# Kernel optimization log

Measured on AMD Instinct MI355X. Metric: run time of the kernel, lower is better.

## Reference

```python
import jax, jax.numpy as jnp
import numpy as np

DIM = 256
HEAD_DIM = 16
HEADS = DIM // HEAD_DIM          # 16
TOTAL = HEADS * HEAD_DIM         # 256
QKV_CH = 3 * TOTAL               # 768
NUM_SCALES = 1
HEADS_TOTAL = HEADS * (1 + NUM_SCALES)  # 32
PROJ_IN = TOTAL * (1 + NUM_SCALES)      # 512
PW_GROUPS = 3 * HEADS            # 48
ATT_EPS = 1e-15
BN_EPS = 1e-5


def _conv(x, w, groups=1, pad=0):
    return jax.lax.conv_general_dilated(
        x, w, window_strides=(1, 1), padding=[(pad, pad), (pad, pad)],
        dimension_numbers=("NCHW", "OIHW", "NCHW"), feature_group_count=groups)


def setup_inputs() -> dict:
    key = jax.random.key(0)
    ks = jax.random.split(key, 9)
    B, H, W = 16, 64, 64
    s = lambda fan: 1.0 / np.sqrt(fan)
    return {
        "x": jax.random.normal(ks[0], (B, DIM, H, W), jnp.float32),
        "w_qkv": jax.random.normal(ks[1], (QKV_CH, DIM, 1, 1), jnp.float32) * s(DIM),
        "w_dw": jax.random.normal(ks[2], (QKV_CH, 1, 5, 5), jnp.float32) * s(25),
        "w_pw": jax.random.normal(ks[3], (QKV_CH, QKV_CH // PW_GROUPS, 1, 1), jnp.float32) * s(QKV_CH // PW_GROUPS),
        "w_proj": jax.random.normal(ks[4], (DIM, PROJ_IN, 1, 1), jnp.float32) * s(PROJ_IN),
        "bn_gamma": jnp.ones((DIM,), jnp.float32),
        "bn_beta": jnp.zeros((DIM,), jnp.float32),
        "bn_mean": jax.random.normal(ks[5], (DIM,), jnp.float32) * 0.1,
        "bn_var": jax.random.uniform(ks[6], (DIM,), jnp.float32, 0.5, 1.5),
    }


def reference(x, w_qkv, w_dw, w_pw, w_proj, bn_gamma, bn_beta, bn_mean, bn_var):
    B, C, H, W = x.shape
    N = H * W
    # qkv projection (1x1 conv, no norm/act)
    qkv = _conv(x, w_qkv)                                   # (B, 768, H, W)
    # multi-scale aggregation: depthwise 5x5 + grouped pointwise
    agg = _conv(_conv(qkv, w_dw, groups=QKV_CH, pad=2), w_pw, groups=PW_GROUPS)
    ms = jnp.concatenate([qkv, agg], axis=1)                # (B, 1536, H, W)
    ms = ms.reshape(B, HEADS_TOTAL, 3 * HEAD_DIM, N)        # (B, 32, 48, N)
    q, k, v = jnp.split(ms, 3, axis=2)                      # each (B, 32, 16, N)
    q = jax.nn.relu(q).astype(jnp.float32)
    k = jax.nn.relu(k).astype(jnp.float32)
    v = v.astype(jnp.float32)
    # pad v with a row of ones -> carries the normalizer through the matmuls
    v_pad = jnp.concatenate([v, jnp.ones((B, HEADS_TOTAL, 1, N), jnp.float32)], axis=2)
    vk = jnp.einsum("bhdn,bhen->bhde", v_pad, k)            # (B, 32, 17, 16)
    out = jnp.einsum("bhde,bhen->bhdn", vk, q)              # (B, 32, 17, N)
    out = out[:, :, :-1] / jnp.clip(out[:, :, -1:], ATT_EPS, None)
    out = out.astype(x.dtype).reshape(B, PROJ_IN, H, W)     # (B, 512, H, W)
    # output projection + BatchNorm (inference stats), no act
    out = _conv(out, w_proj)
    inv = bn_gamma / jnp.sqrt(bn_var + BN_EPS)
    return out * inv[None, :, None, None] + (bn_beta - bn_mean * inv)[None, :, None, None]
```

## Files before the change

kernel.cpp:

```cpp
#include <hip/hip_runtime.h>
#include <math.h>


#define NBC 8

typedef unsigned short u16;
typedef __attribute__((ext_vector_type(8))) short short8v;
typedef __attribute__((ext_vector_type(8))) unsigned short us8;
typedef __attribute__((ext_vector_type(4))) float f32x4;

__device__ __forceinline__ u16 f2bf(float f) {
    union { float f; unsigned u; } v; v.f = f;
    unsigned r = v.u + 0x7fffu + ((v.u >> 16) & 1u);
    return (u16)(r >> 16);
}
__device__ __forceinline__ float bf2f(u16 u) {
    union { unsigned u; float f; } v; v.u = ((unsigned)u) << 16;
    return v.f;
}
__device__ __forceinline__ float4 ld4bf(const u16* p) {
    ushort4 u = *(const ushort4*)p;
    return make_float4(bf2f(u.x), bf2f(u.y), bf2f(u.z), bf2f(u.w));
}

__global__ __launch_bounds__(256) void k_cvt_w(const float* __restrict__ wq,
                                               const float* __restrict__ wp,
                                               u16* __restrict__ wqb, u16* __restrict__ wpb) {
    int i = blockIdx.x * 256 + threadIdx.x;
    if (i < 768 * 256) wqb[i] = f2bf(wq[i]);
    if (i < 256 * 512) wpb[i] = f2bf(wp[i]);
}

__global__ __launch_bounds__(256) void k_tr_x(const float* __restrict__ x,
                                              u16* __restrict__ xbt, int b0) {
    __shared__ u16 t[64][72];
    const int nt = blockIdx.x, ct = blockIdx.y, bb = blockIdx.z;
    const int tid = threadIdx.x;
    const float* xp = x + ((size_t)(b0 + bb) * 256 + ct * 64) * 4096 + nt * 64;
    {
        int cr = tid >> 2, q = tid & 3;
#pragma unroll
        for (int j = 0; j < 4; j++) {
            float4 v = *(const float4*)&xp[(size_t)cr * 4096 + q * 16 + j * 4];
            ushort4 o;
            o.x = f2bf(v.x); o.y = f2bf(v.y); o.z = f2bf(v.z); o.w = f2bf(v.w);
            *(ushort4*)&t[cr][q * 16 + j * 4] = o;
        }
    }
    __syncthreads();
    {
        int nr = tid >> 2, co = (tid & 3) * 16;
        u16* op = xbt + ((size_t)bb * 4096 + nt * 64 + nr) * 256 + ct * 64 + co;
        us8 o0, o1;
#pragma unroll
        for (int j = 0; j < 8; j++) { o0[j] = t[co + j][nr]; o1[j] = t[co + 8 + j][nr]; }
        *(us8*)op = o0;
        *(us8*)(op + 8) = o1;
    }
}

__global__ __launch_bounds__(256) void k_qkv_mm(const u16* __restrict__ xbt,
                                                const u16* __restrict__ wqb,
                                                u16* __restrict__ qkvb) {
    const int bid = blockIdx.x;
    const int mt = bid % 6, nt = bid / 6;
    const int m0 = mt * 128;
    const int cg = nt * 128;
    const int bb = cg >> 12, p0 = cg & 4095;
    const int tid = threadIdx.x, lane = tid & 63, w = tid >> 6;
    const int wm = w >> 1, wn = w & 1;
    const u16* aptr = xbt + ((size_t)bb * 4096 + p0 + wn * 64 + (lane & 15)) * 256 + (lane >> 4) * 8;
    const u16* bptr = wqb + (size_t)(m0 + wm * 64 + (lane & 15)) * 256 + (lane >> 4) * 8;

    f32x4 acc[4][4] = {};
#pragma unroll
    for (int ks = 0; ks < 8; ks++) {
        short8v af[4], bf[4];
#pragma unroll
        for (int i = 0; i < 4; i++) {
            af[i] = *(const short8v*)(aptr + (size_t)i * 16 * 256 + ks * 32);
            bf[i] = *(const short8v*)(bptr + (size_t)i * 16 * 256 + ks * 32);
        }
#pragma unroll
        for (int nf = 0; nf < 4; nf++)
#pragma unroll
            for (int mf = 0; mf < 4; mf++)
                acc[nf][mf] = __builtin_amdgcn_mfma_f32_16x16x32_bf16(af[nf], bf[mf], acc[nf][mf], 0, 0, 0);
    }
    const int mbase = m0 + wm * 64 + (lane & 15);
    const int nbase = p0 + wn * 64 + (lane >> 4) * 4;
#pragma unroll
    for (int nf = 0; nf < 4; nf++)
#pragma unroll
        for (int mf = 0; mf < 4; mf++) {
            int c = mbase + mf * 16;
            int nn = nbase + nf * 16;
            ushort4 o;
            o.x = f2bf(acc[nf][mf][0]);
            o.y = f2bf(acc[nf][mf][1]);
            o.z = f2bf(acc[nf][mf][2]);
            o.w = f2bf(acc[nf][mf][3]);
            *(ushort4*)(qkvb + ((size_t)bb * 768 + c) * 4096 + nn) = o;
        }
}

__global__ __launch_bounds__(256) void k_dwpw(const u16* __restrict__ qkvb,
                                              const float* __restrict__ wdw,
                                              const float* __restrict__ wpw,
                                              u16* __restrict__ aggb) {
    __shared__ float dwt[16 * 4 * 68];
    const int tid = threadIdx.x;
    const int yt = blockIdx.x, g = blockIdx.y, bb = blockIdx.z;
    const int cl = tid >> 4, xq = tid & 15;

    {
        const int c = g * 16 + cl;
        const u16* in = qkvb + ((size_t)bb * 768 + c) * 4096;
        float w[5][5];
#pragma unroll
        for (int dy = 0; dy < 5; dy++)
#pragma unroll
            for (int dx = 0; dx < 5; dx++) w[dy][dx] = wdw[c * 25 + dy * 5 + dx];
        const int x0 = xq * 4;

        float rows[8][8];
#pragma unroll
        for (int r = 0; r < 8; r++) {
            int yy = yt * 4 + r - 2;
            if (yy < 0 || yy > 63) {
#pragma unroll
                for (int j = 0; j < 8; j++) rows[r][j] = 0.f;
            } else {
                const u16* rp = in + yy * 64;
                float4 v0 = (x0 >= 4) ? ld4bf(rp + x0 - 4) : make_float4(0, 0, 0, 0);
                float4 v1 = ld4bf(rp + x0);
                float4 v2 = (x0 + 4 < 64) ? ld4bf(rp + x0 + 4) : make_float4(0, 0, 0, 0);
                rows[r][0] = v0.z; rows[r][1] = v0.w;
                rows[r][2] = v1.x; rows[r][3] = v1.y;
                rows[r][4] = v1.z; rows[r][5] = v1.w;
                rows[r][6] = v2.x; rows[r][7] = v2.y;
            }
        }
#pragma unroll
        for (int ry = 0; ry < 4; ry++) {
            float o0 = 0.f, o1 = 0.f, o2 = 0.f, o3 = 0.f;
#pragma unroll
            for (int dy = 0; dy < 5; dy++) {
#pragma unroll
                for (int dx = 0; dx < 5; dx++) {
                    float wv = w[dy][dx];
                    o0 += rows[ry + dy][0 + dx] * wv;
                    o1 += rows[ry + dy][1 + dx] * wv;
                    o2 += rows[ry + dy][2 + dx] * wv;
                    o3 += rows[ry + dy][3 + dx] * wv;
                }
            }
            float4 ov = make_float4(o0, o1, o2, o3);
            *(float4*)&dwt[(cl * 4 + ry) * 68 + x0] = ov;
        }
    }
    __syncthreads();

    {
        const int oc = cl;
        float wv[16];
#pragma unroll
        for (int ic = 0; ic < 16; ic++)
            wv[ic] = wpw[(size_t)(g * 16 + oc) * 16 + ic];
        const int x0 = xq * 4;
        float acc[4][4];
#pragma unroll
        for (int j = 0; j < 4; j++)
#pragma unroll
            for (int p = 0; p < 4; p++) acc[j][p] = 0.f;
#pragma unroll
        for (int ic = 0; ic < 16; ic++) {
            float wvv = wv[ic];
#pragma unroll
            for (int j = 0; j < 4; j++) {
                float4 f = *(const float4*)&dwt[(ic * 4 + j) * 68 + x0];
                acc[j][0] += wvv * f.x;
                acc[j][1] += wvv * f.y;
                acc[j][2] += wvv * f.z;
                acc[j][3] += wvv * f.w;
            }
        }
        u16* outp = aggb + ((size_t)bb * 768 + g * 16 + oc) * 4096 + yt * 256;
#pragma unroll
        for (int j = 0; j < 4; j++) {
            ushort4 o;
            o.x = f2bf(acc[j][0]);
            o.y = f2bf(acc[j][1]);
            o.z = f2bf(acc[j][2]);
            o.w = f2bf(acc[j][3]);
            *(ushort4*)&outp[j * 64 + x0] = o;
        }
    }
}

__global__ __launch_bounds__(256) void k_vk(const u16* __restrict__ qkvb,
                                            const u16* __restrict__ aggb,
                                            float* __restrict__ gpart) {
    const int h = blockIdx.x, bb = blockIdx.y, ns = blockIdx.z;
    const int tid = threadIdx.x;
    const u16* src = (h < 16) ? qkvb + ((size_t)bb * 768 + h * 48) * 4096
                              : aggb + ((size_t)bb * 768 + (h - 16) * 48) * 4096;
    __shared__ float part[16 * 16 * 17];
    const int e = tid & 15, jg = tid >> 4;
    const int c0 = ns * 512 + jg * 32;
    const u16* kr = src + (size_t)(16 + e) * 4096 + c0;
    const u16* vr = src + (size_t)32 * 4096 + c0;
    float a[17];
#pragma unroll
    for (int d = 0; d < 17; d++) a[d] = 0.f;
#pragma unroll
    for (int i = 0; i < 8; i++) {
        float4 kv = ld4bf(kr + i * 4);
        kv.x = fmaxf(kv.x, 0.f);
        kv.y = fmaxf(kv.y, 0.f);
        kv.z = fmaxf(kv.z, 0.f);
        kv.w = fmaxf(kv.w, 0.f);
#pragma unroll
        for (int d = 0; d < 16; d++) {
            float4 vv = ld4bf(vr + (size_t)d * 4096 + i * 4);
            a[d] += vv.x * kv.x + vv.y * kv.y + vv.z * kv.z + vv.w * kv.w;
        }
        a[16] += kv.x + kv.y + kv.z + kv.w;
    }
#pragma unroll
    for (int d = 0; d < 17; d++) part[(jg * 16 + e) * 17 + d] = a[d];
    __syncthreads();
    for (int idx = tid; idx < 272; idx += 256) {
        int e2 = idx & 15, d2 = idx >> 4;
        float s = 0.f;
#pragma unroll
        for (int j = 0; j < 16; j++) s += part[(j * 16 + e2) * 17 + d2];
        gpart[(((size_t)h * NBC + bb) * 8 + ns) * 272 + idx] = s;
    }
}

__global__ __launch_bounds__(256) void k_att2(const u16* __restrict__ qkvb,
                                              const u16* __restrict__ aggb,
                                              const float* __restrict__ gpart,
                                              u16* __restrict__ attt) {
    const int h = blockIdx.x, bb = blockIdx.y, ns = blockIdx.z;
    const int tid = threadIdx.x;
    const u16* src = (h < 16) ? qkvb + ((size_t)bb * 768 + h * 48) * 4096
                              : aggb + ((size_t)bb * 768 + (h - 16) * 48) * 4096;
    __shared__ float vks[17][16];
    for (int idx = tid; idx < 272; idx += 256) {
        float s = 0.f;
#pragma unroll
        for (int k = 0; k < 8; k++)
            s += gpart[(((size_t)h * NBC + bb) * 8 + k) * 272 + idx];
        vks[idx >> 4][idx & 15] = s;
    }
    __syncthreads();

    const int n = ns * 512 + tid * 2;
    float2 q2[16];
#pragma unroll
    for (int e = 0; e < 16; e++) {
        ushort2 u = *(const ushort2*)(src + (size_t)e * 4096 + n);
        q2[e] = make_float2(fmaxf(bf2f(u.x), 0.f), fmaxf(bf2f(u.y), 0.f));
    }
    float dx = 0.f, dy = 0.f;
#pragma unroll
    for (int e = 0; e < 16; e++) {
        float w = vks[16][e];
        dx += w * q2[e].x;
        dy += w * q2[e].y;
    }
    float rx = 1.f / fmaxf(dx, 1e-15f);
    float ry = 1.f / fmaxf(dy, 1e-15f);
    us8 o0a, o0b, o1a, o1b;
#pragma unroll
    for (int d = 0; d < 16; d++) {
        float ox = 0.f, oy = 0.f;
#pragma unroll
        for (int e = 0; e < 16; e++) {
            float w = vks[d][e];
            ox += w * q2[e].x;
            oy += w * q2[e].y;
        }
        u16 bx = f2bf(ox * rx), by = f2bf(oy * ry);
        if (d < 8) { o0a[d] = bx; o1a[d] = by; }
        else       { o0b[d - 8] = bx; o1b[d - 8] = by; }
    }
    u16* op = attt + ((size_t)bb * 4096 + n) * 512 + h * 16;
    *(us8*)op = o0a;
    *(us8*)(op + 8) = o0b;
    *(us8*)(op + 512) = o1a;
    *(us8*)(op + 520) = o1b;
}

__global__ __launch_bounds__(256) void k_proj_mm(const u16* __restrict__ attt,
                                                 const u16* __restrict__ wpb,
                                                 const float* __restrict__ gamma,
                                                 const float* __restrict__ beta,
                                                 const float* __restrict__ mean,
                                                 const float* __restrict__ var,
                                                 float* __restrict__ out, int b0) {
    const int bid = blockIdx.x;
    const int mt = bid & 1, nt = bid >> 1;
    const int m0 = mt * 128;
    const int cg = nt * 128;
    const int bb = cg >> 12, p0 = cg & 4095;
    const int tid = threadIdx.x, lane = tid & 63, w = tid >> 6;
    const int wm = w >> 1, wn = w & 1;
    const u16* aptr = attt + ((size_t)bb * 4096 + p0 + wn * 64 + (lane & 15)) * 512 + (lane >> 4) * 8;
    const u16* bptr = wpb + (size_t)(m0 + wm * 64 + (lane & 15)) * 512 + (lane >> 4) * 8;

    f32x4 acc[4][4] = {};
#pragma unroll
    for (int ks = 0; ks < 16; ks++) {
        short8v af[4], bf[4];
#pragma unroll
        for (int i = 0; i < 4; i++) {
            af[i] = *(const short8v*)(aptr + (size_t)i * 16 * 512 + ks * 32);
            bf[i] = *(const short8v*)(bptr + (size_t)i * 16 * 512 + ks * 32);
        }
#pragma unroll
        for (int nf = 0; nf < 4; nf++)
#pragma unroll
            for (int mf = 0; mf < 4; mf++)
                acc[nf][mf] = __builtin_amdgcn_mfma_f32_16x16x32_bf16(af[nf], bf[mf], acc[nf][mf], 0, 0, 0);
    }
    const int mbase = m0 + wm * 64 + (lane & 15);
    const int nbase = p0 + wn * 64 + (lane >> 4) * 4;
    float ivv[4], bsv[4];
#pragma unroll
    for (int mf = 0; mf < 4; mf++) {
        int m = mbase + mf * 16;
        float iv = gamma[m] / sqrtf(var[m] + 1e-5f);
        ivv[mf] = iv;
        bsv[mf] = beta[m] - mean[m] * iv;
    }
#pragma unroll
    for (int nf = 0; nf < 4; nf++)
#pragma unroll
        for (int mf = 0; mf < 4; mf++) {
            float4 v;
            v.x = acc[nf][mf][0] * ivv[mf] + bsv[mf];
            v.y = acc[nf][mf][1] * ivv[mf] + bsv[mf];
            v.z = acc[nf][mf][2] * ivv[mf] + bsv[mf];
            v.w = acc[nf][mf][3] * ivv[mf] + bsv[mf];
            *(float4*)(out + ((size_t)(b0 + bb) * 256 + mbase + mf * 16) * 4096 + nbase + nf * 16) = v;
        }
}

extern "C" void kernel_launch(void* const* d_in, const int* in_sizes, int n_in,
                              void* d_out, int out_size, void* d_ws, size_t ws_size,
                              hipStream_t stream) {
    const float* x = (const float*)d_in[0];
    const float* wq = (const float*)d_in[1];
    const float* wdw = (const float*)d_in[2];
    const float* wpw = (const float*)d_in[3];
    const float* wp = (const float*)d_in[4];
    const float* gamma = (const float*)d_in[5];
    const float* beta = (const float*)d_in[6];
    const float* mean = (const float*)d_in[7];
    const float* var = (const float*)d_in[8];
    float* out = (float*)d_out;

    u16* ws = (u16*)d_ws;
    u16* xbt = ws;
    u16* qkvb = xbt + (size_t)NBC * 4096 * 256;
    u16* aggb = qkvb + (size_t)NBC * 768 * 4096;
    u16* attt = aggb + (size_t)NBC * 768 * 4096;
    u16* wqb = attt + (size_t)NBC * 4096 * 512;
    u16* wpb = wqb + 768 * 256;
    float* gpart = (float*)(wpb + 256 * 512);

    k_cvt_w<<<768, 256, 0, stream>>>(wq, wp, wqb, wpb);
    for (int chunk = 0; chunk < 2; ++chunk) {
        int b0 = chunk * NBC;
        k_tr_x<<<dim3(64, 4, NBC), 256, 0, stream>>>(x, xbt, b0);
        k_qkv_mm<<<1536, 256, 0, stream>>>(xbt, wqb, qkvb);
        k_dwpw<<<dim3(16, 48, NBC), 256, 0, stream>>>(qkvb, wdw, wpw, aggb);
        k_vk<<<dim3(32, NBC, 8), 256, 0, stream>>>(qkvb, aggb, gpart);
        k_att2<<<dim3(32, NBC, 8), 256, 0, stream>>>(qkvb, aggb, gpart, attt);
        k_proj_mm<<<512, 256, 0, stream>>>(attt, wpb, gamma, beta, mean, var, out, b0);
    }
}
```

Before: 544.8 us.

## Process 32-row strips per block in dwpw with rolling row buffer

The depthwise+pointwise kernel now has each block sweep 32 output rows in 8 steps, keeping a rolling 8-row register window so each input row is loaded once instead of re-reading the 4-row halo per 4-row tile. Weights are loaded once per block rather than per tile. The grid shrinks from 16 to 2 row-tiles, and a launch bound of 3 blocks per CU is added. The trade-off is fewer blocks (768 per chunk) and two barriers per step, which may reduce latency hiding.

```diff
diff --git a/kernel.cpp b/kernel.cpp
--- a/kernel.cpp
+++ b/kernel.cpp
@@ -104,98 +104,107 @@
         }
 }
 
-__global__ __launch_bounds__(256) void k_dwpw(const u16* __restrict__ qkvb,
-                                              const float* __restrict__ wdw,
-                                              const float* __restrict__ wpw,
-                                              u16* __restrict__ aggb) {
+__global__ __launch_bounds__(256, 3) void k_dwpw(const u16* __restrict__ qkvb,
+                                                 const float* __restrict__ wdw,
+                                                 const float* __restrict__ wpw,
+                                                 u16* __restrict__ aggb) {
     __shared__ float dwt[16 * 4 * 68];
     const int tid = threadIdx.x;
-    const int yt = blockIdx.x, g = blockIdx.y, bb = blockIdx.z;
+    const int ys = blockIdx.x, g = blockIdx.y, bb = blockIdx.z;
     const int cl = tid >> 4, xq = tid & 15;
-
-    {
-        const int c = g * 16 + cl;
-        const u16* in = qkvb + ((size_t)bb * 768 + c) * 4096;
-        float w[5][5];
-#pragma unroll
-        for (int dy = 0; dy < 5; dy++)
-#pragma unroll
-            for (int dx = 0; dx < 5; dx++) w[dy][dx] = wdw[c * 25 + dy * 5 + dx];
-        const int x0 = xq * 4;
-
-        float rows[8][8];
-#pragma unroll
-        for (int r = 0; r < 8; r++) {
-            int yy = yt * 4 + r - 2;
-            if (yy < 0 || yy > 63) {
-#pragma unroll
-                for (int j = 0; j < 8; j++) rows[r][j] = 0.f;
-            } else {
-                const u16* rp = in + yy * 64;
-                float4 v0 = (x0 >= 4) ? ld4bf(rp + x0 - 4) : make_float4(0, 0, 0, 0);
-                float4 v1 = ld4bf(rp + x0);
-                float4 v2 = (x0 + 4 < 64) ? ld4bf(rp + x0 + 4) : make_float4(0, 0, 0, 0);
-                rows[r][0] = v0.z; rows[r][1] = v0.w;
-                rows[r][2] = v1.x; rows[r][3] = v1.y;
-                rows[r][4] = v1.z; rows[r][5] = v1.w;
-                rows[r][6] = v2.x; rows[r][7] = v2.y;
-            }
-        }
+    const int c = g * 16 + cl;
+    const int x0 = xq * 4;
+    const int ybase = ys * 32;
+    const u16* in = qkvb + ((size_t)bb * 768 + c) * 4096;
+    u16* outp0 = aggb + ((size_t)bb * 768 + c) * 4096;
+
+    float w[5][5];
+#pragma unroll
+    for (int dy = 0; dy < 5; dy++)
+#pragma unroll
+        for (int dx = 0; dx < 5; dx++) w[dy][dx] = wdw[c * 25 + dy * 5 + dx];
+    float wv[16];
+#pragma unroll
+    for (int ic = 0; ic < 16; ic++) wv[ic] = wpw[(size_t)c * 16 + ic];
+
+    float rows[8][8];
+
+#define LOADROW(YY, SLOT)                                                     \
+    {                                                                         \
+        int yy_ = (YY);                                                       \
+        if (yy_ < 0 || yy_ > 63) {                                            \
+            _Pragma("unroll") for (int j_ = 0; j_ < 8; j_++) rows[SLOT][j_] = 0.f; \
+        } else {                                                              \
+            const u16* rp_ = in + yy_ * 64;                                   \
+            float4 v0_ = (x0 >= 4) ? ld4bf(rp_ + x0 - 4) : make_float4(0, 0, 0, 0); \
+            float4 v1_ = ld4bf(rp_ + x0);                                     \
+            float4 v2_ = (x0 + 4 < 64) ? ld4bf(rp_ + x0 + 4) : make_float4(0, 0, 0, 0); \
+            rows[SLOT][0] = v0_.z; rows[SLOT][1] = v0_.w;                     \
+            rows[SLOT][2] = v1_.x; rows[SLOT][3] = v1_.y;                     \
+            rows[SLOT][4] = v1_.z; rows[SLOT][5] = v1_.w;                     \
+            rows[SLOT][6] = v2_.x; rows[SLOT][7] = v2_.y;                     \
+        }                                                                     \
+    }
+
+#pragma unroll
+    for (int i = 0; i < 8; i++) LOADROW(ybase - 2 + i, i)
+
+#pragma unroll
+    for (int s = 0; s < 8; s++) {
 #pragma unroll
         for (int ry = 0; ry < 4; ry++) {
             float o0 = 0.f, o1 = 0.f, o2 = 0.f, o3 = 0.f;
 #pragma unroll
             for (int dy = 0; dy < 5; dy++) {
+                const float* rr = rows[(4 * s + ry + dy) & 7];
 #pragma unroll
                 for (int dx = 0; dx < 5; dx++) {
-                    float wv = w[dy][dx];
-                    o0 += rows[ry + dy][0 + dx] * wv;
-                    o1 += rows[ry + dy][1 + dx] * wv;
-                    o2 += rows[ry + dy][2 + dx] * wv;
-                    o3 += rows[ry + dy][3 + dx] * wv;
+                    float wvv = w[dy][dx];
+                    o0 += rr[0 + dx] * wvv;
+                    o1 += rr[1 + dx] * wvv;
+                    o2 += rr[2 + dx] * wvv;
+                    o3 += rr[3 + dx] * wvv;
                 }
             }
             float4 ov = make_float4(o0, o1, o2, o3);
             *(float4*)&dwt[(cl * 4 + ry) * 68 + x0] = ov;
         }
-    }
-    __syncthreads();
-
-    {
-        const int oc = cl;
-        float wv[16];
-#pragma unroll
-        for (int ic = 0; ic < 16; ic++)
-            wv[ic] = wpw[(size_t)(g * 16 + oc) * 16 + ic];
-        const int x0 = xq * 4;
-        float acc[4][4];
-#pragma unroll
-        for (int j = 0; j < 4; j++)
-#pragma unroll
-            for (int p = 0; p < 4; p++) acc[j][p] = 0.f;
-#pragma unroll
-        for (int ic = 0; ic < 16; ic++) {
-            float wvv = wv[ic];
+        if (s < 7) {
+#pragma unroll
+            for (int i = 0; i < 4; i++) LOADROW(ybase + 4 * s + 6 + i, (4 * s + i) & 7)
+        }
+        __syncthreads();
+        {
+            float acc[4][4];
+#pragma unroll
+            for (int j = 0; j < 4; j++)
+#pragma unroll
+                for (int p = 0; p < 4; p++) acc[j][p] = 0.f;
+#pragma unroll
+            for (int ic = 0; ic < 16; ic++) {
+                float wvv = wv[ic];
+#pragma unroll
+                for (int j = 0; j < 4; j++) {
+                    float4 f = *(const float4*)&dwt[(ic * 4 + j) * 68 + x0];
+                    acc[j][0] += wvv * f.x;
+                    acc[j][1] += wvv * f.y;
+                    acc[j][2] += wvv * f.z;
+                    acc[j][3] += wvv * f.w;
+                }
+            }
 #pragma unroll
             for (int j = 0; j < 4; j++) {
-                float4 f = *(const float4*)&dwt[(ic * 4 + j) * 68 + x0];
-                acc[j][0] += wvv * f.x;
-                acc[j][1] += wvv * f.y;
-                acc[j][2] += wvv * f.z;
-                acc[j][3] += wvv * f.w;
+                ushort4 o;
+                o.x = f2bf(acc[j][0]);
+                o.y = f2bf(acc[j][1]);
+                o.z = f2bf(acc[j][2]);
+                o.w = f2bf(acc[j][3]);
+                *(ushort4*)&outp0[(ybase + 4 * s + j) * 64 + x0] = o;
             }
         }
-        u16* outp = aggb + ((size_t)bb * 768 + g * 16 + oc) * 4096 + yt * 256;
-#pragma unroll
-        for (int j = 0; j < 4; j++) {
-            ushort4 o;
-            o.x = f2bf(acc[j][0]);
-            o.y = f2bf(acc[j][1]);
-            o.z = f2bf(acc[j][2]);
-            o.w = f2bf(acc[j][3]);
-            *(ushort4*)&outp[j * 64 + x0] = o;
-        }
-    }
+        __syncthreads();
+    }
+#undef LOADROW
 }
 
 __global__ __launch_bounds__(256) void k_vk(const u16* __restrict__ qkvb,
@@ -377,7 +386,7 @@
         int b0 = chunk * NBC;
         k_tr_x<<<dim3(64, 4, NBC), 256, 0, stream>>>(x, xbt, b0);
         k_qkv_mm<<<1536, 256, 0, stream>>>(xbt, wqb, qkvb);
-        k_dwpw<<<dim3(16, 48, NBC), 256, 0, stream>>>(qkvb, wdw, wpw, aggb);
+        k_dwpw<<<dim3(2, 48, NBC), 256, 0, stream>>>(qkvb, wdw, wpw, aggb);
         k_vk<<<dim3(32, NBC, 8), 256, 0, stream>>>(qkvb, aggb, gpart);
         k_att2<<<dim3(32, NBC, 8), 256, 0, stream>>>(qkvb, aggb, gpart, attt);
         k_proj_mm<<<512, 256, 0, stream>>>(attt, wpb, gamma, beta, mean, var, out, b0);
```

Result: slower. 594.0 us (+9.0%).
